# Kernel optimization log

Measured on AMD Instinct MI355X. Metric: run time of the kernel, lower is better.

Reference implementation:

```python
import jax, jax.numpy as jnp
import numpy as np
from jax import lax

B, C, N, D = 2, 256, 32768, 4
H, W = 256, 256
HW = H * W
NG = 3  # number of 2D grids, cycled across depth


def setup_inputs() -> dict:
    key = jax.random.key(0)
    ks = jax.random.split(key, 8)
    s = 1.0 / np.sqrt(C)
    return {
        "tokens": jax.random.normal(ks[0], (B, C, N), jnp.float32),
        "cell_ind": jax.random.randint(ks[1], (B, NG, N), 0, HW),
        "occupied_cell": jnp.ones((B, N), jnp.float32),
        "cm_gamma": jnp.ones((D, C), jnp.float32),
        "cm_beta": jnp.zeros((D, C), jnp.float32),
        "cm_w1": jax.random.normal(ks[2], (D, C, C), jnp.float32) * s,
        "cm_b1": jnp.zeros((D, C), jnp.float32),
        "cm_w2": jax.random.normal(ks[3], (D, C, C), jnp.float32) * s,
        "cm_b2": jnp.zeros((D, C), jnp.float32),
        "cm_scale": jnp.full((D, C), 1e-2, jnp.float32),
        "sm_gamma": jnp.ones((D, C), jnp.float32),
        "sm_beta": jnp.zeros((D, C), jnp.float32),
        "sm_k1": jax.random.normal(ks[4], (D, C, 3, 3), jnp.float32) / 3.0,
        "sm_b1": jnp.zeros((D, C), jnp.float32),
        "sm_k2": jax.random.normal(ks[5], (D, C, 3, 3), jnp.float32) / 3.0,
        "sm_b2": jnp.zeros((D, C), jnp.float32),
        "sm_scale": jnp.full((D, C), 1e-2, jnp.float32),
    }


def _bn(x, g, b):
    # Training-mode BatchNorm1d: per-channel stats over (batch, points). x: [B,C,N]
    m = jnp.mean(x, axis=(0, 2), keepdims=True)
    v = jnp.mean((x - m) ** 2, axis=(0, 2), keepdims=True)
    return (x - m) * lax.rsqrt(v + 1e-5) * g[None, :, None] + b[None, :, None]


# Per-batch scatter-add of point values into grid cells: vals [N,...], idx [N] -> [HW,...]
_seg = jax.vmap(lambda vals, idx: jax.ops.segment_sum(vals, idx, num_segments=HW))


def _dwconv(x, k, b):
    # Depthwise 3x3 conv. x: [B,H,W,C], k: [C,3,3] (torch groups=C layout)
    kern = jnp.transpose(k, (1, 2, 0))[:, :, None, :]  # [3,3,1,C] HWIO
    y = lax.conv_general_dilated(
        x, kern, (1, 1), "SAME", feature_group_count=C,
        dimension_numbers=("NHWC", "HWIO", "NHWC"))
    return y + b[None, None, None, :]


def reference(tokens, cell_ind, occupied_cell, cm_gamma, cm_beta, cm_w1, cm_b1,
              cm_w2, cm_b2, cm_scale, sm_gamma, sm_beta, sm_k1, sm_b1, sm_k2,
              sm_b2, sm_scale):
    occ = occupied_cell  # [B,N]
    # Precompute per-grid normalized scatter weights (values of the 'flatten' sparse matrix).
    cells, weights = [], []
    for g in range(NG):
        cell = cell_ind[:, g]                                  # [B,N]
        counts = _seg(occ, cell)                               # [B,HW] points per cell
        cnt_pt = jnp.take_along_axis(counts, cell, axis=1) * occ
        cells.append(cell)
        weights.append(occ / (cnt_pt + 1e-6))                  # [B,N]
    for d in range(D):
        cell, w = cells[d % NG], weights[d % NG]
        # --- SpatialMix: scatter -> depthwise-conv FFN -> gather, with LayerScale residual ---
        r = _bn(tokens, sm_gamma[d], sm_beta[d])               # [B,C,N]
        pts = w[:, :, None] * jnp.swapaxes(r, 1, 2)            # [B,N,C]
        grid = _seg(pts, cell).reshape(B, H, W, C)             # flatten: points -> 2D grid
        grid = _dwconv(grid, sm_k1[d], sm_b1[d])
        grid = jax.nn.relu(grid)
        grid = _dwconv(grid, sm_k2[d], sm_b2[d]).reshape(B, HW, C)
        back = occ[:, :, None] * jnp.take_along_axis(grid, cell[:, :, None], axis=1)
        tokens = tokens + sm_scale[d][None, :, None] * jnp.swapaxes(back, 1, 2)
        # --- ChannelMix: BN -> 1x1 MLP -> LayerScale residual ---
        h = _bn(tokens, cm_gamma[d], cm_beta[d])
        h = jnp.einsum("oc,bcn->bon", cm_w1[d], h) + cm_b1[d][None, :, None]
        h = jax.nn.relu(h)
        h = jnp.einsum("oc,bcn->bon", cm_w2[d], h) + cm_b2[d][None, :, None]
        tokens = tokens + cm_scale[d][None, :, None] * h
    return tokens
```

## Files before the change

kernel.cpp:

```cpp
#include <hip/hip_runtime.h>
#include <hip/hip_bf16.h>
#include <stdint.h>

#define BB   2
#define CC   256
#define NN   32768
#define DD   4
#define HH   256
#define WW   256
#define HWC  65536
#define NGG  3

typedef __attribute__((ext_vector_type(8))) short short8;
typedef __attribute__((ext_vector_type(4))) short short4v;
typedef __attribute__((ext_vector_type(4))) float f32x4;

__device__ __forceinline__ short f2bf(float f){
  union { float f; uint32_t u; } v; v.f = f;
  uint32_t u = v.u;
  uint32_t r = (u + 0x7fffu + ((u >> 16) & 1u)) >> 16;
  return (short)r;
}
__device__ __forceinline__ float bf2f(short s){
  union { uint32_t u; float f; } v; v.u = ((uint32_t)(uint16_t)s) << 16;
  return v.f;
}

__global__ __launch_bounds__(256) void count_kernel(const int* cell_ind, const float* occ, float* counts){
  int idx = blockIdx.x * 256 + threadIdx.x;
  int n  = idx & (NN - 1);
  int bg = idx >> 15;
  int b  = bg / NGG;
  atomicAdd(&counts[(size_t)bg * HWC + cell_ind[idx]], occ[(size_t)b * NN + n]);
}

__global__ __launch_bounds__(256) void weight_kernel(const int* cell_ind, const float* occ,
                                                     const float* counts, float* wts){
  int idx = blockIdx.x * 256 + threadIdx.x;
  int n  = idx & (NN - 1);
  int bg = idx >> 15;
  int b  = bg / NGG;
  float o = occ[(size_t)b * NN + n];
  float cnt = counts[(size_t)bg * HWC + cell_ind[idx]];
  wts[idx] = o / (cnt * o + 1e-6f);
}

__global__ __launch_bounds__(256) void bnstats_kernel(const float* tok, const float* gamma,
                                                      const float* beta, float* sOut, float* tOut){
  int c = blockIdx.x;
  int t = threadIdx.x;
  float s = 0.f, sq = 0.f;
  for(int b = 0; b < BB; b++){
    const float4* p = (const float4*)(tok + ((size_t)b * CC + c) * NN);
    for(int i = t; i < NN / 4; i += 256){
      float4 v = p[i];
      s  += v.x + v.y + v.z + v.w;
      sq += v.x * v.x + v.y * v.y + v.z * v.z + v.w * v.w;
    }
  }
  __shared__ float rs[256], rq[256];
  rs[t] = s; rq[t] = sq;
  __syncthreads();
  for(int off = 128; off > 0; off >>= 1){
    if(t < off){ rs[t] += rs[t + off]; rq[t] += rq[t + off]; }
    __syncthreads();
  }
  if(t == 0){
    float m    = rs[0] / (float)(BB * NN);
    float var  = rq[0] / (float)(BB * NN) - m * m;
    float rstd = rsqrtf(var + 1e-5f);
    float g = gamma[c];
    sOut[c] = rstd * g;
    tOut[c] = beta[c] - m * rstd * g;
  }
}

__global__ __launch_bounds__(256) void scatter_kernel(const float* tok, const int* cell_ind,
                                                      const float* wts, const float* sA, const float* tA,
                                                      float* gridA, int g){
  int blk = blockIdx.x;
  int b   = blk >> 9;
  int n0  = (blk & 511) << 6;
  int t   = threadIdx.x;
  __shared__ float lds[256 * 65];
  __shared__ int   cellL[64];
  __shared__ float wL[64];
  if(t < 64){
    cellL[t] = cell_ind[((size_t)b * NGG + g) * NN + n0 + t];
    wL[t]    = wts[((size_t)b * NGG + g) * NN + n0 + t];
  }
  int pf = (t & 15) * 4;
  for(int i = 0; i < 16; i++){
    int c = (t >> 4) + 16 * i;
    float s  = sA[c];
    float tt = tA[c];
    float4 v = *(const float4*)(tok + ((size_t)b * CC + c) * NN + n0 + pf);
    lds[c * 65 + pf + 0] = v.x * s + tt;
    lds[c * 65 + pf + 1] = v.y * s + tt;
    lds[c * 65 + pf + 2] = v.z * s + tt;
    lds[c * 65 + pf + 3] = v.w * s + tt;
  }
  __syncthreads();
  for(int p = 0; p < 64; p++){
    int   cell = cellL[p];
    float wp   = wL[p];
    atomicAdd(&gridA[((size_t)b * HWC + cell) * CC + t], lds[t * 65 + p] * wp);
  }
}

__global__ __launch_bounds__(256) void conv_kernel(const float* __restrict__ gridA,
                                                   const float* __restrict__ k1, const float* __restrict__ b1,
                                                   const float* __restrict__ k2, const float* __restrict__ b2,
                                                   short* __restrict__ gridB){
  int bi = blockIdx.x;
  int tx = bi & 31;
  int ty = (bi >> 5) & 31;
  int b  = bi >> 10;
  int c  = threadIdx.x;
  int x0 = tx * 8, y0 = ty * 8;

  float w1r[9], w2r[9];
  #pragma unroll
  for(int i = 0; i < 9; i++){
    w1r[i] = k1[(size_t)c * 9 + i];
    w2r[i] = k2[(size_t)c * 9 + i];
  }
  float bb1 = b1[c], bb2 = b2[c];

  const float* gb = gridA + (size_t)b * HWC * CC + c;
  short*       ob = gridB + (size_t)b * HWC * CC + c;

  float in[3][12];
  float mid[3][10];

  auto loadrow = [&](int slot, int yy){
    #pragma unroll
    for(int j = 0; j < 12; j++){
      int xx = x0 - 2 + j;
      float v = 0.f;
      if(yy >= 0 && yy < HH && xx >= 0 && xx < WW)
        v = gb[((size_t)yy * WW + xx) * CC];
      in[slot][j] = v;
    }
  };
  loadrow(0, y0 - 2);
  loadrow(1, y0 - 1);

  #pragma unroll
  for(int r = 0; r < 10; r++){
    loadrow((r + 2) % 3, y0 + r);
    int ym = y0 - 1 + r;
    int s0 = r % 3, s1 = (r + 1) % 3, s2 = (r + 2) % 3;
    bool yok = (ym >= 0) && (ym < HH);
    #pragma unroll
    for(int mx = 0; mx < 10; mx++){
      int xg = x0 - 1 + mx;
      float a = bb1;
      #pragma unroll
      for(int kx = 0; kx < 3; kx++){
        a += in[s0][mx + kx] * w1r[0 * 3 + kx];
        a += in[s1][mx + kx] * w1r[1 * 3 + kx];
        a += in[s2][mx + kx] * w1r[2 * 3 + kx];
      }
      float v = fmaxf(a, 0.f);
      if(!yok || xg < 0 || xg >= WW) v = 0.f;
      mid[r % 3][mx] = v;
    }
    if(r >= 2){
      int oy = r - 2;
      int m0 = (r - 2) % 3, m1 = (r - 1) % 3, m2 = r % 3;
      #pragma unroll
      for(int ox = 0; ox < 8; ox++){
        float a = bb2;
        #pragma unroll
        for(int kx = 0; kx < 3; kx++){
          a += mid[m0][ox + kx] * w2r[0 * 3 + kx];
          a += mid[m1][ox + kx] * w2r[1 * 3 + kx];
          a += mid[m2][ox + kx] * w2r[2 * 3 + kx];
        }
        ob[((size_t)(y0 + oy) * WW + (x0 + ox)) * CC] = f2bf(a);
      }
    }
  }
}

__global__ __launch_bounds__(256) void gather_kernel(const float* tokIn, float* tokOut, const short* gridB,
                                                     const int* cell_ind, const float* occ,
                                                     const float* smScale, int g){
  int blk = blockIdx.x;
  int b   = blk >> 9;
  int n0  = (blk & 511) << 6;
  int t   = threadIdx.x;
  __shared__ float lds[256 * 65];
  __shared__ int   cellL[64];
  __shared__ float occL[64];
  if(t < 64){
    cellL[t] = cell_ind[((size_t)b * NGG + g) * NN + n0 + t];
    occL[t]  = occ[(size_t)b * NN + n0 + t];
  }
  __syncthreads();
  int half = t >> 7;
  int ch   = (t & 127) * 2;
  for(int it = 0; it < 32; it++){
    int p = it * 2 + half;
    int cell = cellL[p];
    uint32_t u = *(const uint32_t*)&gridB[((size_t)b * HWC + cell) * CC + ch];
    lds[ch * 65 + p]       = bf2f((short)(u & 0xffff));
    lds[(ch + 1) * 65 + p] = bf2f((short)(u >> 16));
  }
  __syncthreads();
  int pf = (t & 15) * 4;
  for(int i = 0; i < 16; i++){
    int c = (t >> 4) + 16 * i;
    float sc = smScale[c];
    size_t addr = ((size_t)b * CC + c) * NN + n0 + pf;
    float4 tv = *(const float4*)(tokIn + addr);
    float4 o;
    o.x = tv.x + sc * (occL[pf + 0] * lds[c * 65 + pf + 0]);
    o.y = tv.y + sc * (occL[pf + 1] * lds[c * 65 + pf + 1]);
    o.z = tv.z + sc * (occL[pf + 2] * lds[c * 65 + pf + 2]);
    o.w = tv.w + sc * (occL[pf + 3] * lds[c * 65 + pf + 3]);
    *(float4*)(tokOut + addr) = o;
  }
}

__global__ __launch_bounds__(256) void fold_kernel(const float* w1, const float* bias1, const float* w2,
                                                   const float* sB, const float* tB,
                                                   short* W1f, short* W2f, float* b1f){
  int o = blockIdx.x;
  int t = threadIdx.x;
  float w = w1[(size_t)o * CC + t];
  W1f[o * CC + t] = f2bf(w * sB[t]);
  W2f[o * CC + t] = f2bf(w2[(size_t)o * CC + t]);
  __shared__ float red[256];
  red[t] = w * tB[t];
  __syncthreads();
  for(int off = 128; off > 0; off >>= 1){
    if(t < off) red[t] += red[t + off];
    __syncthreads();
  }
  if(t == 0) b1f[o] = bias1[o] + red[0];
}

__global__ __launch_bounds__(256) void mlp_kernel(float* tok, const short* W1f, const float* b1f,
                                                  const short* W2f, const float* b2, const float* sc2){
  int blk = blockIdx.x;
  int b   = blk >> 9;
  int n0  = (blk & 511) << 6;
  int t   = threadIdx.x;
  int w   = t >> 6;
  int l   = t & 63;
  __shared__ short ldsX[64 * 264];
  __shared__ short ldsH[64 * 264];
  float* tb = tok + (size_t)b * CC * NN;

  {
    int nb = t & 15;
    int cbq = t >> 4;
    for(int i = 0; i < 4; i++){
      int c0 = cbq * 4 + 64 * i;
      float4 v0 = *(const float4*)(tb + (size_t)(c0 + 0) * NN + n0 + nb * 4);
      float4 v1 = *(const float4*)(tb + (size_t)(c0 + 1) * NN + n0 + nb * 4);
      float4 v2 = *(const float4*)(tb + (size_t)(c0 + 2) * NN + n0 + nb * 4);
      float4 v3 = *(const float4*)(tb + (size_t)(c0 + 3) * NN + n0 + nb * 4);
      short4v s0 = { f2bf(v0.x), f2bf(v1.x), f2bf(v2.x), f2bf(v3.x) };
      short4v s1 = { f2bf(v0.y), f2bf(v1.y), f2bf(v2.y), f2bf(v3.y) };
      short4v s2 = { f2bf(v0.z), f2bf(v1.z), f2bf(v2.z), f2bf(v3.z) };
      short4v s3 = { f2bf(v0.w), f2bf(v1.w), f2bf(v2.w), f2bf(v3.w) };
      *(short4v*)&ldsX[(nb * 4 + 0) * 264 + c0] = s0;
      *(short4v*)&ldsX[(nb * 4 + 1) * 264 + c0] = s1;
      *(short4v*)&ldsX[(nb * 4 + 2) * 264 + c0] = s2;
      *(short4v*)&ldsX[(nb * 4 + 3) * 264 + c0] = s3;
    }
  }
  __syncthreads();

  int ob = w * 64;
  int lr = l & 15;
  int lq = l >> 4;

  f32x4 acc[4][4];
  for(int m = 0; m < 4; m++)
    for(int nf = 0; nf < 4; nf++)
      acc[m][nf] = (f32x4){0.f, 0.f, 0.f, 0.f};
  for(int kk = 0; kk < 8; kk++){
    int kb = kk * 32 + lq * 8;
    short8 af[4], bfr[4];
    for(int m = 0; m < 4; m++)
      af[m] = *(const short8*)&W1f[(size_t)(ob + m * 16 + lr) * CC + kb];
    for(int nf = 0; nf < 4; nf++)
      bfr[nf] = *(const short8*)&ldsX[(nf * 16 + lr) * 264 + kb];
    for(int m = 0; m < 4; m++)
      for(int nf = 0; nf < 4; nf++)
        acc[m][nf] = __builtin_amdgcn_mfma_f32_16x16x32_bf16(af[m], bfr[nf], acc[m][nf], 0, 0, 0);
  }
  for(int m = 0; m < 4; m++){
    int o0 = ob + m * 16 + lq * 4;
    float bb0 = b1f[o0], bb1 = b1f[o0 + 1], bb2 = b1f[o0 + 2], bb3 = b1f[o0 + 3];
    for(int nf = 0; nf < 4; nf++){
      int n = nf * 16 + lr;
      short4v hv = { f2bf(fmaxf(acc[m][nf][0] + bb0, 0.f)),
                     f2bf(fmaxf(acc[m][nf][1] + bb1, 0.f)),
                     f2bf(fmaxf(acc[m][nf][2] + bb2, 0.f)),
                     f2bf(fmaxf(acc[m][nf][3] + bb3, 0.f)) };
      *(short4v*)&ldsH[n * 264 + o0] = hv;
    }
  }
  __syncthreads();

  f32x4 acc2[4][4];
  for(int m = 0; m < 4; m++)
    for(int nf = 0; nf < 4; nf++)
      acc2[m][nf] = (f32x4){0.f, 0.f, 0.f, 0.f};
  for(int kk = 0; kk < 8; kk++){
    int kb = kk * 32 + lq * 8;
    short8 af[4], bfr[4];
    for(int m = 0; m < 4; m++)
      af[m] = *(const short8*)&W2f[(size_t)(ob + m * 16 + lr) * CC + kb];
    for(int nf = 0; nf < 4; nf++)
      bfr[nf] = *(const short8*)&ldsH[(nf * 16 + lr) * 264 + kb];
    for(int m = 0; m < 4; m++)
      for(int nf = 0; nf < 4; nf++)
        acc2[m][nf] = __builtin_amdgcn_mfma_f32_16x16x32_bf16(af[m], bfr[nf], acc2[m][nf], 0, 0, 0);
  }
  for(int m = 0; m < 4; m++){
    int o0 = ob + m * 16 + lq * 4;
    for(int r = 0; r < 4; r++){
      int o = o0 + r;
      float s  = sc2[o];
      float bb = b2[o];
      for(int nf = 0; nf < 4; nf++){
        int n = nf * 16 + lr;
        size_t addr = (size_t)o * NN + n0 + n;
        tb[addr] = tb[addr] + s * (acc2[m][nf][r] + bb);
      }
    }
  }
}

extern "C" void kernel_launch(void* const* d_in, const int* in_sizes, int n_in,
                              void* d_out, int out_size, void* d_ws, size_t ws_size,
                              hipStream_t stream) {
  const float* tokens   = (const float*)d_in[0];
  const int*   cell_ind = (const int*)d_in[1];
  const float* occ      = (const float*)d_in[2];
  const float* cm_gamma = (const float*)d_in[3];
  const float* cm_beta  = (const float*)d_in[4];
  const float* cm_w1    = (const float*)d_in[5];
  const float* cm_b1    = (const float*)d_in[6];
  const float* cm_w2    = (const float*)d_in[7];
  const float* cm_b2    = (const float*)d_in[8];
  const float* cm_scale = (const float*)d_in[9];
  const float* sm_gamma = (const float*)d_in[10];
  const float* sm_beta  = (const float*)d_in[11];
  const float* sm_k1    = (const float*)d_in[12];
  const float* sm_b1    = (const float*)d_in[13];
  const float* sm_k2    = (const float*)d_in[14];
  const float* sm_b2    = (const float*)d_in[15];
  const float* sm_scale = (const float*)d_in[16];
  float* out = (float*)d_out;
  (void)in_sizes; (void)n_in; (void)out_size; (void)ws_size;

  char* ws = (char*)d_ws;
  size_t off = 0;
  auto carve = [&](size_t bytes) -> void* {
    void* p = ws + off;
    off = (off + bytes + 255) & ~(size_t)255;
    return p;
  };
  float* counts = (float*)carve((size_t)BB * NGG * HWC * 4);
  float* wts    = (float*)carve((size_t)BB * NGG * NN * 4);
  float* sA  = (float*)carve(CC * 4);
  float* tA  = (float*)carve(CC * 4);
  float* sB  = (float*)carve(CC * 4);
  float* tB  = (float*)carve(CC * 4);
  float* b1f = (float*)carve(CC * 4);
  short* W1f = (short*)carve((size_t)CC * CC * 2);
  short* W2f = (short*)carve((size_t)CC * CC * 2);
  float* gridA = (float*)carve((size_t)BB * HWC * CC * 4);
  short* gridB = (short*)carve((size_t)BB * HWC * CC * 2);

  hipMemsetAsync(counts, 0, (size_t)BB * NGG * HWC * 4, stream);
  count_kernel<<<BB * NGG * NN / 256, 256, 0, stream>>>(cell_ind, occ, counts);
  weight_kernel<<<BB * NGG * NN / 256, 256, 0, stream>>>(cell_ind, occ, counts, wts);

  const float* tokCur = tokens;
  for(int d = 0; d < DD; d++){
    int g = d % NGG;
    bnstats_kernel<<<CC, 256, 0, stream>>>(tokCur, sm_gamma + d * CC, sm_beta + d * CC, sA, tA);
    hipMemsetAsync(gridA, 0, (size_t)BB * HWC * CC * 4, stream);
    scatter_kernel<<<BB * NN / 64, 256, 0, stream>>>(tokCur, cell_ind, wts, sA, tA, gridA, g);
    conv_kernel<<<BB * 32 * 32, 256, 0, stream>>>(gridA, sm_k1 + (size_t)d * CC * 9, sm_b1 + d * CC,
                                                  sm_k2 + (size_t)d * CC * 9, sm_b2 + d * CC, gridB);
    gather_kernel<<<BB * NN / 64, 256, 0, stream>>>(tokCur, out, gridB, cell_ind, occ,
                                                    sm_scale + d * CC, g);
    bnstats_kernel<<<CC, 256, 0, stream>>>(out, cm_gamma + d * CC, cm_beta + d * CC, sB, tB);
    fold_kernel<<<CC, 256, 0, stream>>>(cm_w1 + (size_t)d * CC * CC, cm_b1 + d * CC,
                                        cm_w2 + (size_t)d * CC * CC, sB, tB, W1f, W2f, b1f);
    mlp_kernel<<<BB * NN / 64, 256, 0, stream>>>(out, W1f, b1f, W2f, cm_b2 + d * CC, cm_scale + d * CC);
    tokCur = out;
  }
}
```

Baseline: 1.217 ms.

## Fuse BatchNorm statistics into gather and MLP epilogues, swizzle MLP LDS

Channel sums and sums of squares are now accumulated with wave shuffles and atomics inside the gather and MLP kernels. A tiny finalize kernel turns them into BN scale and shift, replacing the separate bnstats passes that re-read the full token tensor. The MLP kernel also uses a single XOR-swizzled LDS buffer shared by X and H instead of two padded buffers. This cuts LDS use and may raise occupancy, at the cost of an extra barrier. Variance is computed as E[x^2]-m^2 with float atomics, so summation order is nondeterministic and precision may be slightly lower.

```diff
diff --git a/kernel.cpp b/kernel.cpp
--- a/kernel.cpp
+++ b/kernel.cpp
@@ -14,6 +14,8 @@
 typedef __attribute__((ext_vector_type(8))) short short8;
 typedef __attribute__((ext_vector_type(4))) short short4v;
 typedef __attribute__((ext_vector_type(4))) float f32x4;
+
+#define LXW(n, c) (((n) << 8) + ((((c) >> 3) ^ ((n) & 7)) << 3) + ((c) & 7))
 
 __device__ __forceinline__ short f2bf(float f){
   union { float f; uint32_t u; } v; v.f = f;
@@ -73,6 +75,20 @@
     sOut[c] = rstd * g;
     tOut[c] = beta[c] - m * rstd * g;
   }
+}
+
+__global__ __launch_bounds__(256) void finalize_kernel(float* mom, const float* gamma, const float* beta,
+                                                       float* sOut, float* tOut){
+  int c = threadIdx.x;
+  const float inv = 1.f / (float)(BB * NN);
+  float m   = mom[c] * inv;
+  float var = mom[256 + c] * inv - m * m;
+  float rstd = rsqrtf(var + 1e-5f);
+  float g = gamma[c];
+  sOut[c] = rstd * g;
+  tOut[c] = beta[c] - m * rstd * g;
+  mom[c] = 0.f;
+  mom[256 + c] = 0.f;
 }
 
 __global__ __launch_bounds__(256) void scatter_kernel(const float* tok, const int* cell_ind,
@@ -186,7 +202,7 @@
 
 __global__ __launch_bounds__(256) void gather_kernel(const float* tokIn, float* tokOut, const short* gridB,
                                                      const int* cell_ind, const float* occ,
-                                                     const float* smScale, int g){
+                                                     const float* smScale, int g, float* cmMom){
   int blk = blockIdx.x;
   int b   = blk >> 9;
   int n0  = (blk & 511) << 6;
@@ -210,6 +226,7 @@
   }
   __syncthreads();
   int pf = (t & 15) * 4;
+  int j  = t & 15;
   for(int i = 0; i < 16; i++){
     int c = (t >> 4) + 16 * i;
     float sc = smScale[c];
@@ -221,6 +238,16 @@
     o.z = tv.z + sc * (occL[pf + 2] * lds[c * 65 + pf + 2]);
     o.w = tv.w + sc * (occL[pf + 3] * lds[c * 65 + pf + 3]);
     *(float4*)(tokOut + addr) = o;
+    float s1 = o.x + o.y + o.z + o.w;
+    float s2 = o.x * o.x + o.y * o.y + o.z * o.z + o.w * o.w;
+    s1 += __shfl_xor(s1, 1);  s2 += __shfl_xor(s2, 1);
+    s1 += __shfl_xor(s1, 2);  s2 += __shfl_xor(s2, 2);
+    s1 += __shfl_xor(s1, 4);  s2 += __shfl_xor(s2, 4);
+    s1 += __shfl_xor(s1, 8);  s2 += __shfl_xor(s2, 8);
+    if(j == (i & 15)){
+      atomicAdd(&cmMom[c], s1);
+      atomicAdd(&cmMom[256 + c], s2);
+    }
   }
 }
 
@@ -243,15 +270,15 @@
 }
 
 __global__ __launch_bounds__(256) void mlp_kernel(float* tok, const short* W1f, const float* b1f,
-                                                  const short* W2f, const float* b2, const float* sc2){
+                                                  const short* W2f, const float* b2, const float* sc2,
+                                                  float* smMom){
   int blk = blockIdx.x;
   int b   = blk >> 9;
   int n0  = (blk & 511) << 6;
   int t   = threadIdx.x;
   int w   = t >> 6;
   int l   = t & 63;
-  __shared__ short ldsX[64 * 264];
-  __shared__ short ldsH[64 * 264];
+  __shared__ short lds[64 * 256];
   float* tb = tok + (size_t)b * CC * NN;
 
   {
@@ -267,10 +294,10 @@
       short4v s1 = { f2bf(v0.y), f2bf(v1.y), f2bf(v2.y), f2bf(v3.y) };
       short4v s2 = { f2bf(v0.z), f2bf(v1.z), f2bf(v2.z), f2bf(v3.z) };
       short4v s3 = { f2bf(v0.w), f2bf(v1.w), f2bf(v2.w), f2bf(v3.w) };
-      *(short4v*)&ldsX[(nb * 4 + 0) * 264 + c0] = s0;
-      *(short4v*)&ldsX[(nb * 4 + 1) * 264 + c0] = s1;
-      *(short4v*)&ldsX[(nb * 4 + 2) * 264 + c0] = s2;
-      *(short4v*)&ldsX[(nb * 4 + 3) * 264 + c0] = s3;
+      *(short4v*)&lds[LXW(nb * 4 + 0, c0)] = s0;
+      *(short4v*)&lds[LXW(nb * 4 + 1, c0)] = s1;
+      *(short4v*)&lds[LXW(nb * 4 + 2, c0)] = s2;
+      *(short4v*)&lds[LXW(nb * 4 + 3, c0)] = s3;
     }
   }
   __syncthreads();
@@ -289,11 +316,13 @@
     for(int m = 0; m < 4; m++)
       af[m] = *(const short8*)&W1f[(size_t)(ob + m * 16 + lr) * CC + kb];
     for(int nf = 0; nf < 4; nf++)
-      bfr[nf] = *(const short8*)&ldsX[(nf * 16 + lr) * 264 + kb];
+      bfr[nf] = *(const short8*)&lds[LXW(nf * 16 + lr, kb)];
     for(int m = 0; m < 4; m++)
       for(int nf = 0; nf < 4; nf++)
         acc[m][nf] = __builtin_amdgcn_mfma_f32_16x16x32_bf16(af[m], bfr[nf], acc[m][nf], 0, 0, 0);
   }
+  __syncthreads();
+
   for(int m = 0; m < 4; m++){
     int o0 = ob + m * 16 + lq * 4;
     float bb0 = b1f[o0], bb1 = b1f[o0 + 1], bb2 = b1f[o0 + 2], bb3 = b1f[o0 + 3];
@@ -303,7 +332,7 @@
                      f2bf(fmaxf(acc[m][nf][1] + bb1, 0.f)),
                      f2bf(fmaxf(acc[m][nf][2] + bb2, 0.f)),
                      f2bf(fmaxf(acc[m][nf][3] + bb3, 0.f)) };
-      *(short4v*)&ldsH[n * 264 + o0] = hv;
+      *(short4v*)&lds[LXW(n, o0)] = hv;
     }
   }
   __syncthreads();
@@ -318,7 +347,7 @@
     for(int m = 0; m < 4; m++)
       af[m] = *(const short8*)&W2f[(size_t)(ob + m * 16 + lr) * CC + kb];
     for(int nf = 0; nf < 4; nf++)
-      bfr[nf] = *(const short8*)&ldsH[(nf * 16 + lr) * 264 + kb];
+      bfr[nf] = *(const short8*)&lds[LXW(nf * 16 + lr, kb)];
     for(int m = 0; m < 4; m++)
       for(int nf = 0; nf < 4; nf++)
         acc2[m][nf] = __builtin_amdgcn_mfma_f32_16x16x32_bf16(af[m], bfr[nf], acc2[m][nf], 0, 0, 0);
@@ -329,10 +358,22 @@
       int o = o0 + r;
       float s  = sc2[o];
       float bb = b2[o];
+      float s1 = 0.f, s2 = 0.f;
       for(int nf = 0; nf < 4; nf++){
         int n = nf * 16 + lr;
         size_t addr = (size_t)o * NN + n0 + n;
-        tb[addr] = tb[addr] + s * (acc2[m][nf][r] + bb);
+        float v = tb[addr] + s * (acc2[m][nf][r] + bb);
+        tb[addr] = v;
+        s1 += v;
+        s2 += v * v;
+      }
+      s1 += __shfl_xor(s1, 1);  s2 += __shfl_xor(s2, 1);
+      s1 += __shfl_xor(s1, 2);  s2 += __shfl_xor(s2, 2);
+      s1 += __shfl_xor(s1, 4);  s2 += __shfl_xor(s2, 4);
+      s1 += __shfl_xor(s1, 8);  s2 += __shfl_xor(s2, 8);
+      if(lr == m * 4 + r){
+        atomicAdd(&smMom[o], s1);
+        atomicAdd(&smMom[256 + o], s2);
       }
     }
   }
@@ -369,6 +410,8 @@
     return p;
   };
   float* counts = (float*)carve((size_t)BB * NGG * HWC * 4);
+  float* smMom  = (float*)carve(512 * 4);
+  float* cmMom  = (float*)carve(512 * 4);
   float* wts    = (float*)carve((size_t)BB * NGG * NN * 4);
   float* sA  = (float*)carve(CC * 4);
   float* tA  = (float*)carve(CC * 4);
@@ -380,24 +423,28 @@
   float* gridA = (float*)carve((size_t)BB * HWC * CC * 4);
   short* gridB = (short*)carve((size_t)BB * HWC * CC * 2);
 
-  hipMemsetAsync(counts, 0, (size_t)BB * NGG * HWC * 4, stream);
+  hipMemsetAsync(counts, 0, (size_t)BB * NGG * HWC * 4 + 2 * 256 * 4 + 512 * 4 + 512 * 4, stream);
   count_kernel<<<BB * NGG * NN / 256, 256, 0, stream>>>(cell_ind, occ, counts);
   weight_kernel<<<BB * NGG * NN / 256, 256, 0, stream>>>(cell_ind, occ, counts, wts);
 
   const float* tokCur = tokens;
   for(int d = 0; d < DD; d++){
     int g = d % NGG;
-    bnstats_kernel<<<CC, 256, 0, stream>>>(tokCur, sm_gamma + d * CC, sm_beta + d * CC, sA, tA);
+    if(d == 0)
+      bnstats_kernel<<<CC, 256, 0, stream>>>(tokCur, sm_gamma, sm_beta, sA, tA);
+    else
+      finalize_kernel<<<1, 256, 0, stream>>>(smMom, sm_gamma + d * CC, sm_beta + d * CC, sA, tA);
     hipMemsetAsync(gridA, 0, (size_t)BB * HWC * CC * 4, stream);
     scatter_kernel<<<BB * NN / 64, 256, 0, stream>>>(tokCur, cell_ind, wts, sA, tA, gridA, g);
     conv_kernel<<<BB * 32 * 32, 256, 0, stream>>>(gridA, sm_k1 + (size_t)d * CC * 9, sm_b1 + d * CC,
                                                   sm_k2 + (size_t)d * CC * 9, sm_b2 + d * CC, gridB);
     gather_kernel<<<BB * NN / 64, 256, 0, stream>>>(tokCur, out, gridB, cell_ind, occ,
-                                                    sm_scale + d * CC, g);
-    bnstats_kernel<<<CC, 256, 0, stream>>>(out, cm_gamma + d * CC, cm_beta + d * CC, sB, tB);
+                                                    sm_scale + d * CC, g, cmMom);
+    finalize_kernel<<<1, 256, 0, stream>>>(cmMom, cm_gamma + d * CC, cm_beta + d * CC, sB, tB);
     fold_kernel<<<CC, 256, 0, stream>>>(cm_w1 + (size_t)d * CC * CC, cm_b1 + d * CC,
                                         cm_w2 + (size_t)d * CC * CC, sB, tB, W1f, W2f, b1f);
-    mlp_kernel<<<BB * NN / 64, 256, 0, stream>>>(out, W1f, b1f, W2f, cm_b2 + d * CC, cm_scale + d * CC);
+    mlp_kernel<<<BB * NN / 64, 256, 0, stream>>>(out, W1f, b1f, W2f, cm_b2 + d * CC,
+                                                 cm_scale + d * CC, smMom);
     tokCur = out;
   }
 }
```

Measured after the change: 1.987 ms. 63.3% more time.
